# Performance work log

Measured on AMD Instinct MI355X. Metric: run time of the kernel, lower is better.

## Reference

```python
import jax, jax.numpy as jnp
import numpy as np

MASK_FILL = -99999.0  # value used by masked_fill_ in the torch source


def setup_inputs() -> dict:
    key = jax.random.key(0)
    k1, k2, k3, k4, k5, k6, k7 = jax.random.split(key, 7)
    B, S, H = 8, 2048, 1024
    query = jax.random.normal(k1, (B, S, H), dtype=jnp.float32)
    key_t = jax.random.normal(k2, (B, S, H), dtype=jnp.float32)
    value = jax.random.normal(k3, (B, S, H), dtype=jnp.float32)
    mask = jax.random.randint(k4, (B, S), 0, 2, dtype=jnp.int32)
    s = 1.0 / np.sqrt(H)
    Wq = jax.random.uniform(k5, (H, H), dtype=jnp.float32, minval=-s, maxval=s)
    Wk = jax.random.uniform(k6, (H, H), dtype=jnp.float32, minval=-s, maxval=s)
    Wv = jax.random.uniform(k7, (H, H), dtype=jnp.float32, minval=-s, maxval=s)
    return {"query": query, "key": key_t, "value": value,
            "Wq": Wq, "Wk": Wk, "Wv": Wv, "mask": mask}


def reference(query, key, value, Wq, Wk, Wv, mask):
    # Linear(h,h,bias=False): y = x @ W.T
    q = jnp.einsum('bsh,oh->bso', query, Wq)
    k = jnp.einsum('bsh,oh->bso', key, Wk)
    v = jnp.einsum('bsh,oh->bso', value, Wv)
    # score[b,i,j] = q[b,i,:] . k[b,j,:]  (NO 1/sqrt(d) scaling in source)
    score = jnp.einsum('bqh,bkh->bqk', q, k)
    # mask: [B, S_k] -> [B, 1, S_k]; positions where mask==0 get MASK_FILL
    m = mask[:, None, :]
    score = jnp.where(m == 0, jnp.float32(MASK_FILL), score)
    attn = jax.nn.softmax(score, axis=-1)
    context = jnp.einsum('bqk,bkh->bqh', attn, v)
    return context
```

## Files before the change

### kernel.cpp

```cpp
#include <hip/hip_runtime.h>
#include <hip/hip_fp16.h>
#include <math.h>

typedef _Float16 f16;
typedef _Float16 f16x4 __attribute__((ext_vector_type(4)));
typedef _Float16 f16x8 __attribute__((ext_vector_type(8)));
typedef float f32x4 __attribute__((ext_vector_type(4)));

#define GLOAD_LDS16(g, l)                                                                  \
    __builtin_amdgcn_global_load_lds((const __attribute__((address_space(1))) void*)(g),   \
                                     (__attribute__((address_space(3))) void*)(l), 16, 0, 0)

__global__ __launch_bounds__(256) void cast3_kernel(const float* __restrict__ s0,
                                                    const float* __restrict__ s1,
                                                    const float* __restrict__ s2,
                                                    f16* d0, f16* d1, f16* d2, int n4each)
{
    const int z = blockIdx.z;
    const float* src = (z == 0) ? s0 : (z == 1) ? s1 : s2;
    f16* d = (z == 0) ? d0 : (z == 1) ? d1 : d2;
    const int stride = gridDim.x * blockDim.x;
    for (int i = blockIdx.x * blockDim.x + threadIdx.x; i < n4each; i += stride) {
        float4 v = *(const float4*)(src + (long long)i * 4);
        *(f16x4*)(d + (long long)i * 4) = (f16x4){(f16)v.x, (f16)v.y, (f16)v.z, (f16)v.w};
    }
}

template <int OUTF16>
__global__ __launch_bounds__(512, 4) void gemm_nt_k(
    const f16* __restrict__ Ab, const f16* __restrict__ Bb, void* __restrict__ Cb,
    int K, int lda, int ldb, int ldc,
    long long sA, long long sB, long long sC, int gx)
{
    __shared__ __align__(16) f16 As[2][256 * 32];
    __shared__ __align__(16) f16 Bs[2][128 * 32];

    const int nwg = gridDim.x;
    const int swz = (blockIdx.x & 7) * (nwg >> 3) + (blockIdx.x >> 3);
    const int bx = swz % gx, by = swz / gx;

    const int z = blockIdx.z;
    const char* pA = (const char*)(Ab + z * sA + (long long)by * 256 * lda);
    const char* pB = (const char*)(Bb + z * sB + (long long)bx * 128 * ldb);
    const long long lda2 = (long long)lda * 2, ldb2 = (long long)ldb * 2;

    const int tid = threadIdx.x;
    const int w = tid >> 6, l = tid & 63;
    const int wr = w >> 1, wc = w & 1;

    const int r0s = tid >> 2;
    const int r1s = 128 + r0s;
    const int cb = (tid & 3) * 16;
    const int c0s = cb ^ ((r0s & 3) << 4);
    const int c1s = cb ^ ((r1s & 3) << 4);

#define STAGE(c, kt)                                                                      \
    do {                                                                                  \
        const long long kb_ = (long long)(kt) * 64;                                       \
        GLOAD_LDS16(pA + (long long)r0s * lda2 + kb_ + c0s, &As[c][(long long)tid * 8]);  \
        GLOAD_LDS16(pA + (long long)r1s * lda2 + kb_ + c1s, &As[c][(512 + (long long)tid) * 8]); \
        GLOAD_LDS16(pB + (long long)r0s * ldb2 + kb_ + c0s, &Bs[c][(long long)tid * 8]);  \
    } while (0)

#define FRAG_A(c, row, kbyte)                                                             \
    (*(const f16x8*)((const char*)&As[c][0] + ((row) * 64) + ((kbyte) ^ (((row) & 3) << 4))))
#define FRAG_B(c, row, kbyte)                                                             \
    (*(const f16x8*)((const char*)&Bs[c][0] + ((row) * 64) + ((kbyte) ^ (((row) & 3) << 4))))

    f32x4 acc[4][4];
#pragma unroll
    for (int i = 0; i < 4; i++)
#pragma unroll
        for (int j = 0; j < 4; j++) acc[i][j] = (f32x4){0.f, 0.f, 0.f, 0.f};

    const int lr = l & 15;
    const int lkb = (l >> 4) * 16;

    const int nt = K >> 5;
    STAGE(0, 0);
    for (int t = 0; t < nt; ++t) {
        const int buf = t & 1;
        if (t + 1 < nt) {
            STAGE(buf ^ 1, t + 1);
            asm volatile("s_waitcnt vmcnt(3)" ::: "memory");
        } else {
            asm volatile("s_waitcnt vmcnt(0)" ::: "memory");
        }
        __builtin_amdgcn_s_barrier();
        __builtin_amdgcn_sched_barrier(0);

        f16x8 bf[4], af[4];
#pragma unroll
        for (int fc = 0; fc < 4; fc++) bf[fc] = FRAG_B(buf, wc * 64 + fc * 16 + lr, lkb);
#pragma unroll
        for (int fq = 0; fq < 4; fq++) af[fq] = FRAG_A(buf, wr * 64 + fq * 16 + lr, lkb);

        __builtin_amdgcn_s_setprio(1);
#pragma unroll
        for (int fq = 0; fq < 4; fq++)
#pragma unroll
            for (int fc = 0; fc < 4; fc++)
                acc[fq][fc] = __builtin_amdgcn_mfma_f32_16x16x32_f16(af[fq], bf[fc], acc[fq][fc], 0, 0, 0);
        __builtin_amdgcn_s_setprio(0);

        __builtin_amdgcn_s_barrier();
        __builtin_amdgcn_sched_barrier(0);
    }
#undef STAGE
#undef FRAG_A
#undef FRAG_B

    const int row_l = (l >> 4) * 4;
    const long long gr0 = (long long)by * 256 + wr * 64;
    const int gc0 = bx * 128 + wc * 64;
    if (OUTF16) {
        f16* C = (f16*)Cb + z * sC;
#pragma unroll
        for (int fq = 0; fq < 4; fq++)
#pragma unroll
            for (int fc = 0; fc < 4; fc++)
#pragma unroll
                for (int i = 0; i < 4; i++)
                    C[(gr0 + fq * 16 + row_l + i) * ldc + gc0 + fc * 16 + lr] = (f16)acc[fq][fc][i];
    } else {
        float* C = (float*)Cb + z * sC;
#pragma unroll
        for (int fq = 0; fq < 4; fq++)
#pragma unroll
            for (int fc = 0; fc < 4; fc++)
#pragma unroll
                for (int i = 0; i < 4; i++)
                    C[(gr0 + fq * 16 + row_l + i) * ldc + gc0 + fc * 16 + lr] = acc[fq][fc][i];
    }
}

__global__ __launch_bounds__(256) void transpose_v_kernel(const f16* __restrict__ v, f16* __restrict__ vT)
{
    __shared__ f16 tile[64][72];
    const int b = blockIdx.z;
    const int s0 = blockIdx.x * 64, o0 = blockIdx.y * 64;
    const int t = threadIdx.x;
    const int r = t >> 2, c = (t & 3) * 16;
    const f16* src = v + ((long long)b * 2048 + s0) * 1024 + o0;
    *(f16x8*)&tile[r][c]     = *(const f16x8*)(src + (long long)r * 1024 + c);
    *(f16x8*)&tile[r][c + 8] = *(const f16x8*)(src + (long long)r * 1024 + c + 8);
    __syncthreads();
    f16* dst = vT + ((long long)b * 1024 + o0) * 2048 + s0;
    f16 buf[16];
#pragma unroll
    for (int j = 0; j < 16; j++) buf[j] = tile[c + j][r];
    *(f16x8*)(dst + (long long)r * 2048 + c)     = *(f16x8*)&buf[0];
    *(f16x8*)(dst + (long long)r * 2048 + c + 8) = *(f16x8*)&buf[8];
}

__device__ __forceinline__ float wred_max(float v) {
#pragma unroll
    for (int o = 32; o > 0; o >>= 1) v = fmaxf(v, __shfl_xor(v, o));
    return v;
}
__device__ __forceinline__ float wred_sum(float v) {
#pragma unroll
    for (int o = 32; o > 0; o >>= 1) v += __shfl_xor(v, o);
    return v;
}

__global__ __launch_bounds__(256) void softmax_kernel(f16* __restrict__ Sm, const int* __restrict__ mask)
{
    const long long row = blockIdx.x;
    const int b = (int)(row >> 11);
    f16* Srow = Sm + row * 2048;
    const int* mrow = mask + b * 2048;
    const int t = threadIdx.x;
    const int w = t >> 6, l = t & 63;

    f16x8 sv = *(const f16x8*)(Srow + t * 8);
    int4 m0 = *(const int4*)(mrow + t * 8);
    int4 m1 = *(const int4*)(mrow + t * 8 + 4);
    int mk[8] = {m0.x, m0.y, m0.z, m0.w, m1.x, m1.y, m1.z, m1.w};
    float v[8];
#pragma unroll
    for (int j = 0; j < 8; j++) v[j] = (float)sv[j];

    float mx = -INFINITY;
#pragma unroll
    for (int j = 0; j < 8; j++) if (mk[j]) mx = fmaxf(mx, v[j]);
    mx = wred_max(mx);
    __shared__ float redm[4], reds[4];
    if (l == 0) redm[w] = mx;
    __syncthreads();
    mx = fmaxf(fmaxf(redm[0], redm[1]), fmaxf(redm[2], redm[3]));

    if (mx == -INFINITY) {
        const f16 u = (f16)(1.0f / 2048.0f);
        f16x8 pv;
#pragma unroll
        for (int j = 0; j < 8; j++) pv[j] = u;
        *(f16x8*)(Srow + t * 8) = pv;
        return;
    }

    float e[8];
    float s = 0.f;
#pragma unroll
    for (int j = 0; j < 8; j++) { e[j] = mk[j] ? expf(v[j] - mx) : 0.f; s += e[j]; }
    s = wred_sum(s);
    if (l == 0) reds[w] = s;
    __syncthreads();
    s = reds[0] + reds[1] + reds[2] + reds[3];
    const float inv = 1.0f / s;
    f16x8 pv;
#pragma unroll
    for (int j = 0; j < 8; j++) pv[j] = (f16)(e[j] * inv);
    *(f16x8*)(Srow + t * 8) = pv;
}

extern "C" void kernel_launch(void* const* d_in, const int* in_sizes, int n_in,
                              void* d_out, int out_size, void* d_ws, size_t ws_size,
                              hipStream_t stream)
{
    const float* query = (const float*)d_in[0];
    const float* keyi  = (const float*)d_in[1];
    const float* value = (const float*)d_in[2];
    const float* Wq    = (const float*)d_in[3];
    const float* Wk    = (const float*)d_in[4];
    const float* Wv    = (const float*)d_in[5];
    const int*   mask  = (const int*)d_in[6];
    float* out = (float*)d_out;

    const long long SH = (long long)8 * 2048 * 1024;
    f16* slot0 = (f16*)d_ws;
    f16* slot1 = slot0 + SH;
    f16* slot2 = slot0 + 2 * SH;
    f16* slot3 = slot0 + 3 * SH;
    f16* slot4 = slot0 + 4 * SH;
    f16* wh    = slot4;
    f16* Pb    = slot0;

    const int n4x = (int)(SH / 4);
    const int n4w = 1024 * 1024 / 4;
    const long long zero = 0;
    const long long M1 = 1024 * 1024;

    cast3_kernel<<<dim3(128, 1, 3), 256, 0, stream>>>(Wq, Wk, Wv, wh, wh + M1, wh + 2 * M1, n4w);
    cast3_kernel<<<dim3(2048, 1, 3), 256, 0, stream>>>(query, keyi, value, slot3, slot0, slot1, n4x);
    gemm_nt_k<1><<<dim3(512, 1, 1), 512, 0, stream>>>(
        slot3, wh, (void*)slot2, 1024, 1024, 1024, 1024, zero, zero, zero, 8);
    gemm_nt_k<1><<<dim3(512, 1, 1), 512, 0, stream>>>(
        slot0, wh + M1, (void*)slot3, 1024, 1024, 1024, 1024, zero, zero, zero, 8);
    gemm_nt_k<1><<<dim3(512, 1, 1), 512, 0, stream>>>(
        slot1, wh + 2 * M1, (void*)slot0, 1024, 1024, 1024, 1024, zero, zero, zero, 8);
    transpose_v_kernel<<<dim3(32, 16, 8), 256, 0, stream>>>(slot0, slot4);
    gemm_nt_k<1><<<dim3(128, 1, 8), 512, 0, stream>>>(
        slot2, slot3, (void*)Pb, 1024, 1024, 1024, 2048,
        (long long)2048 * 1024, (long long)2048 * 1024, (long long)2048 * 2048, 16);
    softmax_kernel<<<dim3(16384), 256, 0, stream>>>(Pb, mask);
    gemm_nt_k<0><<<dim3(64, 1, 8), 512, 0, stream>>>(
        Pb, slot4, (void*)out, 2048, 2048, 2048, 1024,
        (long long)2048 * 2048, (long long)1024 * 2048, (long long)2048 * 1024, 8);
}
```

Measured before the change: 380.2 us.

## Replace double-buffered K=32 GEMM pipeline with single-buffered K=64 tiles

The GEMM main loop drops LDS double buffering with explicit vmcnt waits and prefetch of the next tile. It now loads a K=64 slice into one buffer per iteration and synchronises with __syncthreads before and after compute. The LDS swizzle widens to 8 rows, the launch-bounds occupancy hint drops from 4 to 2, and the setprio hints are removed. This halves the number of barriers per K and doubles the MFMA work per sync, but global loads no longer overlap with compute.

```diff
diff --git a/kernel.cpp b/kernel.cpp
--- a/kernel.cpp
+++ b/kernel.cpp
@@ -27,13 +27,13 @@
 }
 
 template <int OUTF16>
-__global__ __launch_bounds__(512, 4) void gemm_nt_k(
+__global__ __launch_bounds__(512, 2) void gemm_nt_k(
     const f16* __restrict__ Ab, const f16* __restrict__ Bb, void* __restrict__ Cb,
     int K, int lda, int ldb, int ldc,
     long long sA, long long sB, long long sC, int gx)
 {
-    __shared__ __align__(16) f16 As[2][256 * 32];
-    __shared__ __align__(16) f16 Bs[2][128 * 32];
+    __shared__ __align__(16) f16 As[256 * 64];
+    __shared__ __align__(16) f16 Bs[128 * 64];
 
     const int nwg = gridDim.x;
     const int swz = (blockIdx.x & 7) * (nwg >> 3) + (blockIdx.x >> 3);
@@ -48,25 +48,6 @@
     const int w = tid >> 6, l = tid & 63;
     const int wr = w >> 1, wc = w & 1;
 
-    const int r0s = tid >> 2;
-    const int r1s = 128 + r0s;
-    const int cb = (tid & 3) * 16;
-    const int c0s = cb ^ ((r0s & 3) << 4);
-    const int c1s = cb ^ ((r1s & 3) << 4);
-
-#define STAGE(c, kt)                                                                      \
-    do {                                                                                  \
-        const long long kb_ = (long long)(kt) * 64;                                       \
-        GLOAD_LDS16(pA + (long long)r0s * lda2 + kb_ + c0s, &As[c][(long long)tid * 8]);  \
-        GLOAD_LDS16(pA + (long long)r1s * lda2 + kb_ + c1s, &As[c][(512 + (long long)tid) * 8]); \
-        GLOAD_LDS16(pB + (long long)r0s * ldb2 + kb_ + c0s, &Bs[c][(long long)tid * 8]);  \
-    } while (0)
-
-#define FRAG_A(c, row, kbyte)                                                             \
-    (*(const f16x8*)((const char*)&As[c][0] + ((row) * 64) + ((kbyte) ^ (((row) & 3) << 4))))
-#define FRAG_B(c, row, kbyte)                                                             \
-    (*(const f16x8*)((const char*)&Bs[c][0] + ((row) * 64) + ((kbyte) ^ (((row) & 3) << 4))))
-
     f32x4 acc[4][4];
 #pragma unroll
     for (int i = 0; i < 4; i++)
@@ -76,37 +57,53 @@
     const int lr = l & 15;
     const int lkb = (l >> 4) * 16;
 
-    const int nt = K >> 5;
-    STAGE(0, 0);
+#define FRAG_A(row, kbyte)                                                                \
+    (*(const f16x8*)((const char*)&As[0] + ((row) * 128) + ((kbyte) ^ (((row) & 7) << 4))))
+#define FRAG_B(row, kbyte)                                                                \
+    (*(const f16x8*)((const char*)&Bs[0] + ((row) * 128) + ((kbyte) ^ (((row) & 7) << 4))))
+
+    const int nt = K >> 6;
     for (int t = 0; t < nt; ++t) {
-        const int buf = t & 1;
-        if (t + 1 < nt) {
-            STAGE(buf ^ 1, t + 1);
-            asm volatile("s_waitcnt vmcnt(3)" ::: "memory");
-        } else {
-            asm volatile("s_waitcnt vmcnt(0)" ::: "memory");
+        const long long kb = (long long)t * 128;
+#pragma unroll
+        for (int i = 0; i < 4; i++) {
+            const int c = i * 512 + tid;
+            const int row = c >> 3;
+            const int col = ((c & 7) * 16) ^ ((row & 7) << 4);
+            GLOAD_LDS16(pA + (long long)row * lda2 + kb + col, &As[(long long)c * 8]);
         }
-        __builtin_amdgcn_s_barrier();
-        __builtin_amdgcn_sched_barrier(0);
-
-        f16x8 bf[4], af[4];
-#pragma unroll
-        for (int fc = 0; fc < 4; fc++) bf[fc] = FRAG_B(buf, wc * 64 + fc * 16 + lr, lkb);
-#pragma unroll
-        for (int fq = 0; fq < 4; fq++) af[fq] = FRAG_A(buf, wr * 64 + fq * 16 + lr, lkb);
-
-        __builtin_amdgcn_s_setprio(1);
+#pragma unroll
+        for (int i = 0; i < 2; i++) {
+            const int c = i * 512 + tid;
+            const int row = c >> 3;
+            const int col = ((c & 7) * 16) ^ ((row & 7) << 4);
+            GLOAD_LDS16(pB + (long long)row * ldb2 + kb + col, &Bs[(long long)c * 8]);
+        }
+        __syncthreads();
+
+        f16x8 bf[4][2], af[4][2];
+#pragma unroll
+        for (int fc = 0; fc < 4; fc++)
+#pragma unroll
+            for (int ks = 0; ks < 2; ks++)
+                bf[fc][ks] = FRAG_B(wc * 64 + fc * 16 + lr, ks * 64 + lkb);
+#pragma unroll
+        for (int fq = 0; fq < 4; fq++)
+#pragma unroll
+            for (int ks = 0; ks < 2; ks++)
+                af[fq][ks] = FRAG_A(wr * 64 + fq * 16 + lr, ks * 64 + lkb);
+
 #pragma unroll
         for (int fq = 0; fq < 4; fq++)
 #pragma unroll
             for (int fc = 0; fc < 4; fc++)
-                acc[fq][fc] = __builtin_amdgcn_mfma_f32_16x16x32_f16(af[fq], bf[fc], acc[fq][fc], 0, 0, 0);
-        __builtin_amdgcn_s_setprio(0);
-
-        __builtin_amdgcn_s_barrier();
-        __builtin_amdgcn_sched_barrier(0);
-    }
-#undef STAGE
+#pragma unroll
+                for (int ks = 0; ks < 2; ks++)
+                    acc[fq][fc] = __builtin_amdgcn_mfma_f32_16x16x32_f16(
+                        af[fq][ks], bf[fc][ks], acc[fq][fc], 0, 0, 0);
+
+        __syncthreads();
+    }
 #undef FRAG_A
 #undef FRAG_B
 
```

New measurement: 332.6 us. -12.5%, faster.
